# Performance work log

Measured on AMD Instinct MI355X. Metric: run time of the kernel, lower is better.

Reference implementation:

```python
import jax, jax.numpy as jnp
import numpy as np

N = 8192        # nodes
NFEAT = 256     # input feature dim
NHID = 64       # per-head hidden dim
NHEADS = 4
NCLASS = 121    # PPI label count
ALPHA = 0.2     # LeakyReLU negative slope
NEG_INF = jnp.float32(-9e15)  # pyGAT's mask fill value


def setup_inputs() -> dict:
    key = jax.random.key(0)
    k = jax.random.split(key, 6)
    x = jax.random.normal(k[0], (N, NFEAT), dtype=jnp.float32)
    adj = (jax.random.uniform(k[1], (N, N)) < 0.01).astype(jnp.float32)
    idx = jnp.arange(N)
    adj = adj.at[idx, idx].set(1.0)
    # per-head first-layer params: W [H, nfeat, nhid], a [H, 2*nhid]
    Ws = jax.random.normal(k[2], (NHEADS, NFEAT, NHID), dtype=jnp.float32) * 0.1
    a_heads = jax.random.normal(k[3], (NHEADS, 2 * NHID), dtype=jnp.float32) * 0.1
    # output attention layer params
    W_out = jax.random.normal(k[4], (NHEADS * NHID, NCLASS), dtype=jnp.float32) * 0.1
    a_out = jax.random.normal(k[5], (2 * NCLASS,), dtype=jnp.float32) * 0.1
    return {"x": x, "adj": adj, "Ws": Ws, "a_heads": a_heads,
            "W_out": W_out, "a_out": a_out}


def _gat_head(x, adj, W, a, concat):
    # Dense GraphAttentionLayer (pyGAT), eval mode (dropout off).
    Wh = x @ W                                   # [N, d]
    d = W.shape[1]
    f_src = Wh @ a[:d]                           # [N]  score contribution of node i
    f_dst = Wh @ a[d:]                           # [N]  score contribution of node j
    e = jax.nn.leaky_relu(f_src[:, None] + f_dst[None, :], ALPHA)  # [N, N]
    e = jnp.where(adj > 0, e, NEG_INF)
    att = jax.nn.softmax(e, axis=-1)             # [N, N]
    h = att @ Wh                                 # [N, d]
    return jax.nn.elu(h) if concat else h


def reference(x, adj, Ws, a_heads, W_out, a_out):
    # first multi-head layer (concat=True, elu), vmapped over heads
    heads = jax.vmap(lambda W, a: _gat_head(x, adj, W, a, True))(Ws, a_heads)  # [H, N, nhid]
    h_cat = jnp.transpose(heads, (1, 0, 2)).reshape(x.shape[0], NHEADS * NHID)  # torch.cat(dim=1)
    # output attention layer (concat=False -> raw aggregation)
    return _gat_head(h_cat, adj, W_out, a_out, False)  # [N, nclass]
```

## Files before the change

### kernel.cpp

```cpp
#include <hip/hip_runtime.h>
#include <math.h>

#define N_NODES 8192
#define NFEAT 256
#define NHID 64
#define NHEADS 4
#define NCLASS 121
#define NCPAD 128
#define CAP 256
#define LRALPHA 0.2f

__global__ __launch_bounds__(256) void build_csr(const float* __restrict__ adj,
                                                 int* __restrict__ nbr,
                                                 int* __restrict__ deg) {
    int row = blockIdx.x;
    __shared__ int cnt;
    if (threadIdx.x == 0) cnt = 0;
    __syncthreads();
    const float4* arow = (const float4*)(adj + (size_t)row * N_NODES);
    for (int j4 = threadIdx.x; j4 < N_NODES / 4; j4 += 256) {
        float4 v = arow[j4];
        if (v.x > 0.f) { int s = atomicAdd(&cnt, 1); if (s < CAP) nbr[row * CAP + s] = j4 * 4 + 0; }
        if (v.y > 0.f) { int s = atomicAdd(&cnt, 1); if (s < CAP) nbr[row * CAP + s] = j4 * 4 + 1; }
        if (v.z > 0.f) { int s = atomicAdd(&cnt, 1); if (s < CAP) nbr[row * CAP + s] = j4 * 4 + 2; }
        if (v.w > 0.f) { int s = atomicAdd(&cnt, 1); if (s < CAP) nbr[row * CAP + s] = j4 * 4 + 3; }
    }
    __syncthreads();
    if (threadIdx.x == 0) deg[row] = cnt < CAP ? cnt : CAP;
}

__global__ __launch_bounds__(256) void pad_params(const float* __restrict__ Wout,
                                                  const float* __restrict__ aout,
                                                  float* __restrict__ Wpad,
                                                  float* __restrict__ apad) {
    int idx = blockIdx.x * 256 + threadIdx.x;
    if (idx < 256 * NCPAD) {
        int k = idx >> 7, c = idx & 127;
        Wpad[idx] = (c < NCLASS) ? Wout[k * NCLASS + c] : 0.f;
    }
    if (idx < 256) {
        int c = idx & 127;
        float v = 0.f;
        if (c < NCLASS) v = (idx < 128) ? aout[c] : aout[NCLASS + c];
        apad[idx] = v;
    }
}

__global__ __launch_bounds__(256) void gemm1(const float* __restrict__ x,
                                             const float* __restrict__ Ws,
                                             float* __restrict__ Wh1) {
    int h = blockIdx.y;
    int r0 = blockIdx.x * 64;
    __shared__ float xs[64][260];
    for (int t = threadIdx.x; t < 64 * 64; t += 256) {
        int r = t >> 6, c4 = t & 63;
        *(float4*)&xs[r][c4 * 4] = *(const float4*)(x + (size_t)(r0 + r) * NFEAT + c4 * 4);
    }
    __syncthreads();
    int d = threadIdx.x & 63;
    int rb = (threadIdx.x >> 6) * 16;
    const float* W = Ws + (size_t)h * NFEAT * NHID + d;
    float acc[16] = {};
    for (int k4 = 0; k4 < NFEAT; k4 += 4) {
        float b0 = W[(k4 + 0) * NHID];
        float b1 = W[(k4 + 1) * NHID];
        float b2 = W[(k4 + 2) * NHID];
        float b3 = W[(k4 + 3) * NHID];
#pragma unroll
        for (int r = 0; r < 16; r++) {
            float4 a = *(const float4*)&xs[rb + r][k4];
            acc[r] += a.x * b0 + a.y * b1 + a.z * b2 + a.w * b3;
        }
    }
#pragma unroll
    for (int r = 0; r < 16; r++)
        Wh1[((size_t)(r0 + rb + r) * NHEADS + h) * NHID + d] = acc[r];
}

__global__ __launch_bounds__(256) void attn_coef1(const float* __restrict__ Wh1,
                                                  const float* __restrict__ a_heads,
                                                  float* __restrict__ fs1,
                                                  float* __restrict__ fd1) {
    int i = blockIdx.x;
    int h = threadIdx.x >> 6, lane = threadIdx.x & 63;
    float wh = Wh1[((size_t)i * NHEADS + h) * NHID + lane];
    float s = wh * a_heads[h * 2 * NHID + lane];
    float dd = wh * a_heads[h * 2 * NHID + NHID + lane];
#pragma unroll
    for (int o = 32; o > 0; o >>= 1) { s += __shfl_down(s, o); dd += __shfl_down(dd, o); }
    if (lane == 0) { fs1[h * N_NODES + i] = s; fd1[h * N_NODES + i] = dd; }
}

__global__ __launch_bounds__(256) void attn_agg1(const int* __restrict__ nbr,
                                                 const int* __restrict__ deg,
                                                 const float* __restrict__ Wh1,
                                                 const float* __restrict__ fs1,
                                                 const float* __restrict__ fd1,
                                                 float* __restrict__ hcat) {
    int i = blockIdx.x;
    int h = threadIdx.x >> 6, lane = threadIdx.x & 63;
    __shared__ float ebuf[NHEADS][CAP];
    __shared__ int nbrs[CAP];
    int dg = deg[i];
    for (int t = threadIdx.x; t < dg; t += 256) nbrs[t] = nbr[i * CAP + t];
    __syncthreads();
    float fsi = fs1[h * N_NODES + i];
    const float* fdh = fd1 + h * N_NODES;
    float m = -3.4e38f;
    for (int t = lane; t < dg; t += 64) {
        float e = fsi + fdh[nbrs[t]];
        e = e > 0.f ? e : LRALPHA * e;
        ebuf[h][t] = e;
        m = fmaxf(m, e);
    }
#pragma unroll
    for (int o = 32; o > 0; o >>= 1) m = fmaxf(m, __shfl_xor(m, o));
    float s = 0.f;
    for (int t = lane; t < dg; t += 64) {
        float p = __expf(ebuf[h][t] - m);
        ebuf[h][t] = p;
        s += p;
    }
#pragma unroll
    for (int o = 32; o > 0; o >>= 1) s += __shfl_xor(s, o);
    __syncthreads();
    float acc = 0.f;
    const float* whh = Wh1 + h * NHID + lane;
    for (int t = 0; t < dg; t++) {
        int j = nbrs[t];
        acc += ebuf[h][t] * whh[(size_t)j * (NHEADS * NHID)];
    }
    acc /= s;
    float r = acc > 0.f ? acc : expm1f(acc);
    hcat[(size_t)i * (NHEADS * NHID) + h * NHID + lane] = r;
}

__global__ __launch_bounds__(256) void gemm2(const float* __restrict__ hcat,
                                             const float* __restrict__ Wpad,
                                             float* __restrict__ Wh2) {
    int r0 = blockIdx.x * 64;
    __shared__ float xs[64][260];
    for (int t = threadIdx.x; t < 64 * 64; t += 256) {
        int r = t >> 6, c4 = t & 63;
        *(float4*)&xs[r][c4 * 4] = *(const float4*)(hcat + (size_t)(r0 + r) * 256 + c4 * 4);
    }
    __syncthreads();
    int c0 = (threadIdx.x & 63) * 2;
    int rb = (threadIdx.x >> 6) * 16;
    float acc0[16] = {}, acc1[16] = {};
    for (int k4 = 0; k4 < 256; k4 += 4) {
        float2 b0 = *(const float2*)&Wpad[(k4 + 0) * NCPAD + c0];
        float2 b1 = *(const float2*)&Wpad[(k4 + 1) * NCPAD + c0];
        float2 b2 = *(const float2*)&Wpad[(k4 + 2) * NCPAD + c0];
        float2 b3 = *(const float2*)&Wpad[(k4 + 3) * NCPAD + c0];
#pragma unroll
        for (int r = 0; r < 16; r++) {
            float4 a = *(const float4*)&xs[rb + r][k4];
            acc0[r] += a.x * b0.x + a.y * b1.x + a.z * b2.x + a.w * b3.x;
            acc1[r] += a.x * b0.y + a.y * b1.y + a.z * b2.y + a.w * b3.y;
        }
    }
#pragma unroll
    for (int r = 0; r < 16; r++) {
        float2 v = make_float2(acc0[r], acc1[r]);
        *(float2*)&Wh2[(size_t)(r0 + rb + r) * NCPAD + c0] = v;
    }
}

__global__ __launch_bounds__(256) void attn_coef2(const float* __restrict__ Wh2,
                                                  const float* __restrict__ apad,
                                                  float* __restrict__ fs2,
                                                  float* __restrict__ fd2) {
    int i = blockIdx.x * 4 + (threadIdx.x >> 6);
    int lane = threadIdx.x & 63;
    float w0 = Wh2[(size_t)i * NCPAD + lane];
    float w1 = Wh2[(size_t)i * NCPAD + 64 + lane];
    float s = w0 * apad[lane] + w1 * apad[64 + lane];
    float dd = w0 * apad[128 + lane] + w1 * apad[192 + lane];
#pragma unroll
    for (int o = 32; o > 0; o >>= 1) { s += __shfl_down(s, o); dd += __shfl_down(dd, o); }
    if (lane == 0) { fs2[i] = s; fd2[i] = dd; }
}

__global__ __launch_bounds__(128) void attn_agg2(const int* __restrict__ nbr,
                                                 const int* __restrict__ deg,
                                                 const float* __restrict__ Wh2,
                                                 const float* __restrict__ fs2,
                                                 const float* __restrict__ fd2,
                                                 float* __restrict__ out) {
    int i = blockIdx.x;
    int t = threadIdx.x;
    __shared__ float ebuf[CAP];
    __shared__ int nbrs[CAP];
    __shared__ float red[2];
    int dg = deg[i];
    for (int u = t; u < dg; u += 128) nbrs[u] = nbr[i * CAP + u];
    __syncthreads();
    float fsi = fs2[i];
    float m = -3.4e38f;
    for (int u = t; u < dg; u += 128) {
        float e = fsi + fd2[nbrs[u]];
        e = e > 0.f ? e : LRALPHA * e;
        ebuf[u] = e;
        m = fmaxf(m, e);
    }
#pragma unroll
    for (int o = 32; o > 0; o >>= 1) m = fmaxf(m, __shfl_xor(m, o));
    if ((t & 63) == 0) red[t >> 6] = m;
    __syncthreads();
    m = fmaxf(red[0], red[1]);
    float s = 0.f;
    for (int u = t; u < dg; u += 128) {
        float p = __expf(ebuf[u] - m);
        ebuf[u] = p;
        s += p;
    }
#pragma unroll
    for (int o = 32; o > 0; o >>= 1) s += __shfl_xor(s, o);
    __syncthreads();
    if ((t & 63) == 0) red[t >> 6] = s;
    __syncthreads();
    s = red[0] + red[1];
    float acc = 0.f;
    const float* wcol = Wh2 + t;
    for (int u = 0; u < dg; u++) {
        acc += ebuf[u] * wcol[(size_t)nbrs[u] * NCPAD];
    }
    if (t < NCLASS) out[(size_t)i * NCLASS + t] = acc / s;
}


extern "C" void kernel_launch(void* const* d_in, const int* in_sizes, int n_in,
                              void* d_out, int out_size, void* d_ws, size_t ws_size,
                              hipStream_t stream) {
    const float* x       = (const float*)d_in[0];
    const float* adj     = (const float*)d_in[1];
    const float* Ws      = (const float*)d_in[2];
    const float* a_heads = (const float*)d_in[3];
    const float* Wout    = (const float*)d_in[4];
    const float* aout    = (const float*)d_in[5];
    float* out = (float*)d_out;

    char* ws = (char*)d_ws;
    size_t off = 0;
    auto alloc = [&](size_t bytes) { void* p = ws + off; off = (off + bytes + 255) & ~(size_t)255; return p; };
    int*   nbr  = (int*)  alloc((size_t)N_NODES * CAP * 4);
    int*   deg  = (int*)  alloc((size_t)N_NODES * 4);
    float* Wh1  = (float*)alloc((size_t)N_NODES * NHEADS * NHID * 4);
    float* fs1  = (float*)alloc((size_t)NHEADS * N_NODES * 4);
    float* fd1  = (float*)alloc((size_t)NHEADS * N_NODES * 4);
    float* hcat = (float*)alloc((size_t)N_NODES * NHEADS * NHID * 4);
    float* Wh2  = (float*)alloc((size_t)N_NODES * NCPAD * 4);
    float* fs2  = (float*)alloc((size_t)N_NODES * 4);
    float* fd2  = (float*)alloc((size_t)N_NODES * 4);
    float* Wpad = (float*)alloc((size_t)256 * NCPAD * 4);
    float* apad = (float*)alloc((size_t)256 * 4);

    build_csr<<<N_NODES, 256, 0, stream>>>(adj, nbr, deg);
    pad_params<<<128, 256, 0, stream>>>(Wout, aout, Wpad, apad);
    gemm1<<<dim3(N_NODES / 64, NHEADS), 256, 0, stream>>>(x, Ws, Wh1);
    attn_coef1<<<N_NODES, 256, 0, stream>>>(Wh1, a_heads, fs1, fd1);
    attn_agg1<<<N_NODES, 256, 0, stream>>>(nbr, deg, Wh1, fs1, fd1, hcat);
    gemm2<<<N_NODES / 64, 256, 0, stream>>>(hcat, Wpad, Wh2);
    attn_coef2<<<N_NODES / 4, 256, 0, stream>>>(Wh2, apad, fs2, fd2);
    attn_agg2<<<N_NODES, 128, 0, stream>>>(nbr, deg, Wh2, fs2, fd2, out);
}
```

Measured before the change: 528.1 us.

## Store per-head feature matrices contiguously and remap aggregation blocks to one head

Wh1 and Wh2 are now stored head-major (and column-half-major for layer 2), so each gathered neighbour row is a contiguous 256-byte segment. The aggregation kernels are remapped so that each block covers four nodes for a single head or column half, with one wavefront per node. This keeps the gathered table for one head small enough to stay cache-resident. Non-temporal loads and stores are added for the adjacency scan, the neighbour lists and the outputs to reduce cache pollution. The cost is more redundant neighbour-list loads per node across heads, and the rewritten blocks depend on a correct block-index remapping.

Result: faster. 509.1 us (-3.6%).

```diff
diff --git a/kernel.cpp b/kernel.cpp
--- a/kernel.cpp
+++ b/kernel.cpp
@@ -10,6 +10,8 @@
 #define CAP 256
 #define LRALPHA 0.2f
 
+typedef float f32x4 __attribute__((ext_vector_type(4)));
+
 __global__ __launch_bounds__(256) void build_csr(const float* __restrict__ adj,
                                                  int* __restrict__ nbr,
                                                  int* __restrict__ deg) {
@@ -17,9 +19,9 @@
     __shared__ int cnt;
     if (threadIdx.x == 0) cnt = 0;
     __syncthreads();
-    const float4* arow = (const float4*)(adj + (size_t)row * N_NODES);
+    const f32x4* arow = (const f32x4*)(adj + (size_t)row * N_NODES);
     for (int j4 = threadIdx.x; j4 < N_NODES / 4; j4 += 256) {
-        float4 v = arow[j4];
+        f32x4 v = __builtin_nontemporal_load(&arow[j4]);
         if (v.x > 0.f) { int s = atomicAdd(&cnt, 1); if (s < CAP) nbr[row * CAP + s] = j4 * 4 + 0; }
         if (v.y > 0.f) { int s = atomicAdd(&cnt, 1); if (s < CAP) nbr[row * CAP + s] = j4 * 4 + 1; }
         if (v.z > 0.f) { int s = atomicAdd(&cnt, 1); if (s < CAP) nbr[row * CAP + s] = j4 * 4 + 2; }
@@ -48,7 +50,7 @@
 
 __global__ __launch_bounds__(256) void gemm1(const float* __restrict__ x,
                                              const float* __restrict__ Ws,
-                                             float* __restrict__ Wh1) {
+                                             float* __restrict__ Wh1h) {
     int h = blockIdx.y;
     int r0 = blockIdx.x * 64;
     __shared__ float xs[64][260];
@@ -74,16 +76,16 @@
     }
 #pragma unroll
     for (int r = 0; r < 16; r++)
-        Wh1[((size_t)(r0 + rb + r) * NHEADS + h) * NHID + d] = acc[r];
-}
-
-__global__ __launch_bounds__(256) void attn_coef1(const float* __restrict__ Wh1,
+        Wh1h[((size_t)h * N_NODES + (r0 + rb + r)) * NHID + d] = acc[r];
+}
+
+__global__ __launch_bounds__(256) void attn_coef1(const float* __restrict__ Wh1h,
                                                   const float* __restrict__ a_heads,
                                                   float* __restrict__ fs1,
                                                   float* __restrict__ fd1) {
     int i = blockIdx.x;
     int h = threadIdx.x >> 6, lane = threadIdx.x & 63;
-    float wh = Wh1[((size_t)i * NHEADS + h) * NHID + lane];
+    float wh = Wh1h[((size_t)h * N_NODES + i) * NHID + lane];
     float s = wh * a_heads[h * 2 * NHID + lane];
     float dd = wh * a_heads[h * 2 * NHID + NHID + lane];
 #pragma unroll
@@ -93,51 +95,55 @@
 
 __global__ __launch_bounds__(256) void attn_agg1(const int* __restrict__ nbr,
                                                  const int* __restrict__ deg,
-                                                 const float* __restrict__ Wh1,
+                                                 const float* __restrict__ Wh1h,
                                                  const float* __restrict__ fs1,
                                                  const float* __restrict__ fd1,
                                                  float* __restrict__ hcat) {
-    int i = blockIdx.x;
-    int h = threadIdx.x >> 6, lane = threadIdx.x & 63;
-    __shared__ float ebuf[NHEADS][CAP];
-    __shared__ int nbrs[CAP];
+    int b = blockIdx.x;
+    int w = threadIdx.x >> 6, lane = threadIdx.x & 63;
+    int slot = b & 7;
+    int h = slot >> 1;
+    int g = ((b >> 3) << 1) | (slot & 1);
+    int i = (g << 2) | w;
+    __shared__ float ebuf[4][CAP];
+    __shared__ int nbrs[4][CAP];
     int dg = deg[i];
-    for (int t = threadIdx.x; t < dg; t += 256) nbrs[t] = nbr[i * CAP + t];
-    __syncthreads();
+    for (int t = lane; t < dg; t += 64)
+        nbrs[w][t] = __builtin_nontemporal_load(&nbr[i * CAP + t]);
     float fsi = fs1[h * N_NODES + i];
     const float* fdh = fd1 + h * N_NODES;
     float m = -3.4e38f;
     for (int t = lane; t < dg; t += 64) {
-        float e = fsi + fdh[nbrs[t]];
+        float e = fsi + fdh[nbrs[w][t]];
         e = e > 0.f ? e : LRALPHA * e;
-        ebuf[h][t] = e;
+        ebuf[w][t] = e;
         m = fmaxf(m, e);
     }
 #pragma unroll
     for (int o = 32; o > 0; o >>= 1) m = fmaxf(m, __shfl_xor(m, o));
     float s = 0.f;
     for (int t = lane; t < dg; t += 64) {
-        float p = __expf(ebuf[h][t] - m);
-        ebuf[h][t] = p;
+        float p = __expf(ebuf[w][t] - m);
+        ebuf[w][t] = p;
         s += p;
     }
 #pragma unroll
     for (int o = 32; o > 0; o >>= 1) s += __shfl_xor(s, o);
     __syncthreads();
     float acc = 0.f;
-    const float* whh = Wh1 + h * NHID + lane;
+    const float* wcol = Wh1h + (size_t)h * N_NODES * NHID + lane;
+#pragma unroll 4
     for (int t = 0; t < dg; t++) {
-        int j = nbrs[t];
-        acc += ebuf[h][t] * whh[(size_t)j * (NHEADS * NHID)];
+        acc += ebuf[w][t] * wcol[(size_t)nbrs[w][t] * NHID];
     }
     acc /= s;
     float r = acc > 0.f ? acc : expm1f(acc);
-    hcat[(size_t)i * (NHEADS * NHID) + h * NHID + lane] = r;
+    __builtin_nontemporal_store(r, &hcat[(size_t)i * (NHEADS * NHID) + h * NHID + lane]);
 }
 
 __global__ __launch_bounds__(256) void gemm2(const float* __restrict__ hcat,
                                              const float* __restrict__ Wpad,
-                                             float* __restrict__ Wh2) {
+                                             float* __restrict__ Wh2h) {
     int r0 = blockIdx.x * 64;
     __shared__ float xs[64][260];
     for (int t = threadIdx.x; t < 64 * 64; t += 256) {
@@ -147,6 +153,7 @@
     __syncthreads();
     int c0 = (threadIdx.x & 63) * 2;
     int rb = (threadIdx.x >> 6) * 16;
+    int half = c0 >> 6, cc = c0 & 63;
     float acc0[16] = {}, acc1[16] = {};
     for (int k4 = 0; k4 < 256; k4 += 4) {
         float2 b0 = *(const float2*)&Wpad[(k4 + 0) * NCPAD + c0];
@@ -163,18 +170,18 @@
 #pragma unroll
     for (int r = 0; r < 16; r++) {
         float2 v = make_float2(acc0[r], acc1[r]);
-        *(float2*)&Wh2[(size_t)(r0 + rb + r) * NCPAD + c0] = v;
-    }
-}
-
-__global__ __launch_bounds__(256) void attn_coef2(const float* __restrict__ Wh2,
+        *(float2*)&Wh2h[((size_t)half * N_NODES + (r0 + rb + r)) * 64 + cc] = v;
+    }
+}
+
+__global__ __launch_bounds__(256) void attn_coef2(const float* __restrict__ Wh2h,
                                                   const float* __restrict__ apad,
                                                   float* __restrict__ fs2,
                                                   float* __restrict__ fd2) {
     int i = blockIdx.x * 4 + (threadIdx.x >> 6);
     int lane = threadIdx.x & 63;
-    float w0 = Wh2[(size_t)i * NCPAD + lane];
-    float w1 = Wh2[(size_t)i * NCPAD + 64 + lane];
+    float w0 = Wh2h[(size_t)i * 64 + lane];
+    float w1 = Wh2h[((size_t)N_NODES + i) * 64 + lane];
     float s = w0 * apad[lane] + w1 * apad[64 + lane];
     float dd = w0 * apad[128 + lane] + w1 * apad[192 + lane];
 #pragma unroll
@@ -182,51 +189,51 @@
     if (lane == 0) { fs2[i] = s; fd2[i] = dd; }
 }
 
-__global__ __launch_bounds__(128) void attn_agg2(const int* __restrict__ nbr,
+__global__ __launch_bounds__(256) void attn_agg2(const int* __restrict__ nbr,
                                                  const int* __restrict__ deg,
-                                                 const float* __restrict__ Wh2,
+                                                 const float* __restrict__ Wh2h,
                                                  const float* __restrict__ fs2,
                                                  const float* __restrict__ fd2,
                                                  float* __restrict__ out) {
-    int i = blockIdx.x;
-    int t = threadIdx.x;
-    __shared__ float ebuf[CAP];
-    __shared__ int nbrs[CAP];
-    __shared__ float red[2];
+    int b = blockIdx.x;
+    int w = threadIdx.x >> 6, lane = threadIdx.x & 63;
+    int slot = b & 7;
+    int hf = slot >> 2;
+    int g = ((b >> 3) << 2) | (slot & 3);
+    int i = (g << 2) | w;
+    __shared__ float ebuf[4][CAP];
+    __shared__ int nbrs[4][CAP];
     int dg = deg[i];
-    for (int u = t; u < dg; u += 128) nbrs[u] = nbr[i * CAP + u];
-    __syncthreads();
+    for (int t = lane; t < dg; t += 64)
+        nbrs[w][t] = __builtin_nontemporal_load(&nbr[i * CAP + t]);
     float fsi = fs2[i];
     float m = -3.4e38f;
-    for (int u = t; u < dg; u += 128) {
-        float e = fsi + fd2[nbrs[u]];
+    for (int t = lane; t < dg; t += 64) {
+        float e = fsi + fd2[nbrs[w][t]];
         e = e > 0.f ? e : LRALPHA * e;
-        ebuf[u] = e;
+        ebuf[w][t] = e;
         m = fmaxf(m, e);
     }
 #pragma unroll
     for (int o = 32; o > 0; o >>= 1) m = fmaxf(m, __shfl_xor(m, o));
-    if ((t & 63) == 0) red[t >> 6] = m;
-    __syncthreads();
-    m = fmaxf(red[0], red[1]);
     float s = 0.f;
-    for (int u = t; u < dg; u += 128) {
-        float p = __expf(ebuf[u] - m);
-        ebuf[u] = p;
+    for (int t = lane; t < dg; t += 64) {
+        float p = __expf(ebuf[w][t] - m);
+        ebuf[w][t] = p;
         s += p;
     }
 #pragma unroll
     for (int o = 32; o > 0; o >>= 1) s += __shfl_xor(s, o);
     __syncthreads();
-    if ((t & 63) == 0) red[t >> 6] = s;
-    __syncthreads();
-    s = red[0] + red[1];
     float acc = 0.f;
-    const float* wcol = Wh2 + t;
-    for (int u = 0; u < dg; u++) {
-        acc += ebuf[u] * wcol[(size_t)nbrs[u] * NCPAD];
-    }
-    if (t < NCLASS) out[(size_t)i * NCLASS + t] = acc / s;
+    const float* wcol = Wh2h + (size_t)hf * N_NODES * 64 + lane;
+#pragma unroll 4
+    for (int t = 0; t < dg; t++) {
+        acc += ebuf[w][t] * wcol[(size_t)nbrs[w][t] * 64];
+    }
+    int c = hf * 64 + lane;
+    if (c < NCLASS)
+        __builtin_nontemporal_store(acc / s, &out[(size_t)i * NCLASS + c]);
 }
 
 
@@ -246,11 +253,11 @@
     auto alloc = [&](size_t bytes) { void* p = ws + off; off = (off + bytes + 255) & ~(size_t)255; return p; };
     int*   nbr  = (int*)  alloc((size_t)N_NODES * CAP * 4);
     int*   deg  = (int*)  alloc((size_t)N_NODES * 4);
-    float* Wh1  = (float*)alloc((size_t)N_NODES * NHEADS * NHID * 4);
+    float* Wh1h = (float*)alloc((size_t)NHEADS * N_NODES * NHID * 4);
     float* fs1  = (float*)alloc((size_t)NHEADS * N_NODES * 4);
     float* fd1  = (float*)alloc((size_t)NHEADS * N_NODES * 4);
     float* hcat = (float*)alloc((size_t)N_NODES * NHEADS * NHID * 4);
-    float* Wh2  = (float*)alloc((size_t)N_NODES * NCPAD * 4);
+    float* Wh2h = (float*)alloc((size_t)2 * N_NODES * 64 * 4);
     float* fs2  = (float*)alloc((size_t)N_NODES * 4);
     float* fd2  = (float*)alloc((size_t)N_NODES * 4);
     float* Wpad = (float*)alloc((size_t)256 * NCPAD * 4);
@@ -258,10 +265,10 @@
 
     build_csr<<<N_NODES, 256, 0, stream>>>(adj, nbr, deg);
     pad_params<<<128, 256, 0, stream>>>(Wout, aout, Wpad, apad);
-    gemm1<<<dim3(N_NODES / 64, NHEADS), 256, 0, stream>>>(x, Ws, Wh1);
-    attn_coef1<<<N_NODES, 256, 0, stream>>>(Wh1, a_heads, fs1, fd1);
-    attn_agg1<<<N_NODES, 256, 0, stream>>>(nbr, deg, Wh1, fs1, fd1, hcat);
-    gemm2<<<N_NODES / 64, 256, 0, stream>>>(hcat, Wpad, Wh2);
-    attn_coef2<<<N_NODES / 4, 256, 0, stream>>>(Wh2, apad, fs2, fd2);
-    attn_agg2<<<N_NODES, 128, 0, stream>>>(nbr, deg, Wh2, fs2, fd2, out);
-}
+    gemm1<<<dim3(N_NODES / 64, NHEADS), 256, 0, stream>>>(x, Ws, Wh1h);
+    attn_coef1<<<N_NODES, 256, 0, stream>>>(Wh1h, a_heads, fs1, fd1);
+    attn_agg1<<<N_NODES, 256, 0, stream>>>(nbr, deg, Wh1h, fs1, fd1, hcat);
+    gemm2<<<N_NODES / 64, 256, 0, stream>>>(hcat, Wpad, Wh2h);
+    attn_coef2<<<N_NODES / 4, 256, 0, stream>>>(Wh2h, apad, fs2, fd2);
+    attn_agg2<<<N_NODES / 2, 256, 0, stream>>>(nbr, deg, Wh2h, fs2, fd2, out);
+}
```

## Restructure attention aggregation to one wavefront per node with vectorized gathers

Applied to the files above, without the earlier changes.

Both aggregation kernels now give each 64-lane wavefront one node (four nodes per block) instead of one block per node. The first layer handles all four heads at once, using head-interleaved fs/fd arrays and float4 gathers of neighbor features. The output layer splits neighbors across two half-waves that combine with a shuffle. The adjacency scan in build_csr uses nontemporal loads. The intent is to cut block-level syncs, raise memory-level parallelism and use wider loads in the gather-bound phases. The cost is more register pressure and a hard limit of four neighbor chunks per lane, which matches CAP=256.

Result: faster. 485.2 us (-8.1%).

```diff
diff --git a/kernel.cpp b/kernel.cpp
--- a/kernel.cpp
+++ b/kernel.cpp
@@ -10,6 +10,11 @@
 #define CAP 256
 #define LRALPHA 0.2f
 
+typedef float f32x4 __attribute__((ext_vector_type(4)));
+
+__device__ __forceinline__ float lrelu(float x) { return x > 0.f ? x : LRALPHA * x; }
+__device__ __forceinline__ f32x4 splat4(float v) { f32x4 r = {v, v, v, v}; return r; }
+
 __global__ __launch_bounds__(256) void build_csr(const float* __restrict__ adj,
                                                  int* __restrict__ nbr,
                                                  int* __restrict__ deg) {
@@ -17,9 +22,9 @@
     __shared__ int cnt;
     if (threadIdx.x == 0) cnt = 0;
     __syncthreads();
-    const float4* arow = (const float4*)(adj + (size_t)row * N_NODES);
+    const f32x4* arow = (const f32x4*)(adj + (size_t)row * N_NODES);
     for (int j4 = threadIdx.x; j4 < N_NODES / 4; j4 += 256) {
-        float4 v = arow[j4];
+        f32x4 v = __builtin_nontemporal_load(&arow[j4]);
         if (v.x > 0.f) { int s = atomicAdd(&cnt, 1); if (s < CAP) nbr[row * CAP + s] = j4 * 4 + 0; }
         if (v.y > 0.f) { int s = atomicAdd(&cnt, 1); if (s < CAP) nbr[row * CAP + s] = j4 * 4 + 1; }
         if (v.z > 0.f) { int s = atomicAdd(&cnt, 1); if (s < CAP) nbr[row * CAP + s] = j4 * 4 + 2; }
@@ -74,65 +79,101 @@
     }
 #pragma unroll
     for (int r = 0; r < 16; r++)
-        Wh1[((size_t)(r0 + rb + r) * NHEADS + h) * NHID + d] = acc[r];
+        Wh1[(size_t)(r0 + rb + r) * (NHEADS * NHID) + h * NHID + d] = acc[r];
 }
 
 __global__ __launch_bounds__(256) void attn_coef1(const float* __restrict__ Wh1,
                                                   const float* __restrict__ a_heads,
-                                                  float* __restrict__ fs1,
-                                                  float* __restrict__ fd1) {
+                                                  float* __restrict__ fs1t,
+                                                  float* __restrict__ fd1t) {
     int i = blockIdx.x;
     int h = threadIdx.x >> 6, lane = threadIdx.x & 63;
-    float wh = Wh1[((size_t)i * NHEADS + h) * NHID + lane];
+    float wh = Wh1[(size_t)i * (NHEADS * NHID) + h * NHID + lane];
     float s = wh * a_heads[h * 2 * NHID + lane];
     float dd = wh * a_heads[h * 2 * NHID + NHID + lane];
 #pragma unroll
     for (int o = 32; o > 0; o >>= 1) { s += __shfl_down(s, o); dd += __shfl_down(dd, o); }
-    if (lane == 0) { fs1[h * N_NODES + i] = s; fd1[h * N_NODES + i] = dd; }
+    if (lane == 0) { fs1t[i * 4 + h] = s; fd1t[i * 4 + h] = dd; }
 }
 
 __global__ __launch_bounds__(256) void attn_agg1(const int* __restrict__ nbr,
                                                  const int* __restrict__ deg,
                                                  const float* __restrict__ Wh1,
-                                                 const float* __restrict__ fs1,
-                                                 const float* __restrict__ fd1,
+                                                 const float* __restrict__ fs1t,
+                                                 const float* __restrict__ fd1t,
                                                  float* __restrict__ hcat) {
-    int i = blockIdx.x;
-    int h = threadIdx.x >> 6, lane = threadIdx.x & 63;
-    __shared__ float ebuf[NHEADS][CAP];
-    __shared__ int nbrs[CAP];
+    int w = threadIdx.x >> 6, lane = threadIdx.x & 63;
+    int i = blockIdx.x * 4 + w;
+    __shared__ int nbrs[4][CAP];
+    __shared__ float pbuf[4][CAP][4];
     int dg = deg[i];
-    for (int t = threadIdx.x; t < dg; t += 256) nbrs[t] = nbr[i * CAP + t];
-    __syncthreads();
-    float fsi = fs1[h * N_NODES + i];
-    const float* fdh = fd1 + h * N_NODES;
-    float m = -3.4e38f;
-    for (int t = lane; t < dg; t += 64) {
-        float e = fsi + fdh[nbrs[t]];
-        e = e > 0.f ? e : LRALPHA * e;
-        ebuf[h][t] = e;
-        m = fmaxf(m, e);
-    }
-#pragma unroll
-    for (int o = 32; o > 0; o >>= 1) m = fmaxf(m, __shfl_xor(m, o));
-    float s = 0.f;
-    for (int t = lane; t < dg; t += 64) {
-        float p = __expf(ebuf[h][t] - m);
-        ebuf[h][t] = p;
-        s += p;
-    }
-#pragma unroll
-    for (int o = 32; o > 0; o >>= 1) s += __shfl_xor(s, o);
-    __syncthreads();
-    float acc = 0.f;
-    const float* whh = Wh1 + h * NHID + lane;
+    for (int t = lane; t < dg; t += 64)
+        nbrs[w][t] = nbr[i * CAP + t];
+    f32x4 fsi = *(const f32x4*)(fs1t + (size_t)i * 4);
+    f32x4 e[4];
+    f32x4 m4 = {-3.4e38f, -3.4e38f, -3.4e38f, -3.4e38f};
+#pragma unroll
+    for (int k = 0; k < 4; k++) {
+        int t = lane + (k << 6);
+        if (t < dg) {
+            int j = nbrs[w][t];
+            f32x4 fdj = *(const f32x4*)(fd1t + (size_t)j * 4);
+            f32x4 ev;
+            ev.x = lrelu(fsi.x + fdj.x);
+            ev.y = lrelu(fsi.y + fdj.y);
+            ev.z = lrelu(fsi.z + fdj.z);
+            ev.w = lrelu(fsi.w + fdj.w);
+            e[k] = ev;
+            m4.x = fmaxf(m4.x, ev.x); m4.y = fmaxf(m4.y, ev.y);
+            m4.z = fmaxf(m4.z, ev.z); m4.w = fmaxf(m4.w, ev.w);
+        }
+    }
+#pragma unroll
+    for (int o = 32; o > 0; o >>= 1) {
+        m4.x = fmaxf(m4.x, __shfl_xor(m4.x, o));
+        m4.y = fmaxf(m4.y, __shfl_xor(m4.y, o));
+        m4.z = fmaxf(m4.z, __shfl_xor(m4.z, o));
+        m4.w = fmaxf(m4.w, __shfl_xor(m4.w, o));
+    }
+    f32x4 s4 = {0.f, 0.f, 0.f, 0.f};
+#pragma unroll
+    for (int k = 0; k < 4; k++) {
+        int t = lane + (k << 6);
+        if (t < dg) {
+            f32x4 p;
+            p.x = __expf(e[k].x - m4.x);
+            p.y = __expf(e[k].y - m4.y);
+            p.z = __expf(e[k].z - m4.z);
+            p.w = __expf(e[k].w - m4.w);
+            *(f32x4*)&pbuf[w][t][0] = p;
+            s4 += p;
+        }
+    }
+#pragma unroll
+    for (int o = 32; o > 0; o >>= 1) {
+        s4.x += __shfl_xor(s4.x, o);
+        s4.y += __shfl_xor(s4.y, o);
+        s4.z += __shfl_xor(s4.z, o);
+        s4.w += __shfl_xor(s4.w, o);
+    }
+    __syncthreads();
+    int hl = lane >> 4;
+    const float* wrow = Wh1 + 4 * lane;
+    f32x4 acc = {0.f, 0.f, 0.f, 0.f};
+#pragma unroll 4
     for (int t = 0; t < dg; t++) {
-        int j = nbrs[t];
-        acc += ebuf[h][t] * whh[(size_t)j * (NHEADS * NHID)];
-    }
-    acc /= s;
-    float r = acc > 0.f ? acc : expm1f(acc);
-    hcat[(size_t)i * (NHEADS * NHID) + h * NHID + lane] = r;
+        int j = nbrs[w][t];
+        float p = pbuf[w][t][hl];
+        f32x4 wv = *(const f32x4*)(wrow + (size_t)j * (NHEADS * NHID));
+        acc += wv * splat4(p);
+    }
+    float sh = hl == 0 ? s4.x : hl == 1 ? s4.y : hl == 2 ? s4.z : s4.w;
+    acc.x /= sh; acc.y /= sh; acc.z /= sh; acc.w /= sh;
+    acc.x = acc.x > 0.f ? acc.x : expm1f(acc.x);
+    acc.y = acc.y > 0.f ? acc.y : expm1f(acc.y);
+    acc.z = acc.z > 0.f ? acc.z : expm1f(acc.z);
+    acc.w = acc.w > 0.f ? acc.w : expm1f(acc.w);
+    *(f32x4*)(hcat + (size_t)i * (NHEADS * NHID) + 4 * lane) = acc;
 }
 
 __global__ __launch_bounds__(256) void gemm2(const float* __restrict__ hcat,
@@ -182,51 +223,67 @@
     if (lane == 0) { fs2[i] = s; fd2[i] = dd; }
 }
 
-__global__ __launch_bounds__(128) void attn_agg2(const int* __restrict__ nbr,
+__global__ __launch_bounds__(256) void attn_agg2(const int* __restrict__ nbr,
                                                  const int* __restrict__ deg,
                                                  const float* __restrict__ Wh2,
                                                  const float* __restrict__ fs2,
                                                  const float* __restrict__ fd2,
                                                  float* __restrict__ out) {
-    int i = blockIdx.x;
-    int t = threadIdx.x;
-    __shared__ float ebuf[CAP];
-    __shared__ int nbrs[CAP];
-    __shared__ float red[2];
+    int w = threadIdx.x >> 6, lane = threadIdx.x & 63;
+    int i = blockIdx.x * 4 + w;
+    __shared__ int nbrs[4][CAP];
+    __shared__ float pbuf[4][CAP];
     int dg = deg[i];
-    for (int u = t; u < dg; u += 128) nbrs[u] = nbr[i * CAP + u];
-    __syncthreads();
+    for (int t = lane; t < dg; t += 64)
+        nbrs[w][t] = nbr[i * CAP + t];
     float fsi = fs2[i];
+    float e[4];
     float m = -3.4e38f;
-    for (int u = t; u < dg; u += 128) {
-        float e = fsi + fd2[nbrs[u]];
-        e = e > 0.f ? e : LRALPHA * e;
-        ebuf[u] = e;
-        m = fmaxf(m, e);
+#pragma unroll
+    for (int k = 0; k < 4; k++) {
+        int t = lane + (k << 6);
+        if (t < dg) {
+            float ev = lrelu(fsi + fd2[nbrs[w][t]]);
+            e[k] = ev;
+            m = fmaxf(m, ev);
+        }
     }
 #pragma unroll
     for (int o = 32; o > 0; o >>= 1) m = fmaxf(m, __shfl_xor(m, o));
-    if ((t & 63) == 0) red[t >> 6] = m;
-    __syncthreads();
-    m = fmaxf(red[0], red[1]);
     float s = 0.f;
-    for (int u = t; u < dg; u += 128) {
-        float p = __expf(ebuf[u] - m);
-        ebuf[u] = p;
-        s += p;
+#pragma unroll
+    for (int k = 0; k < 4; k++) {
+        int t = lane + (k << 6);
+        if (t < dg) {
+            float p = __expf(e[k] - m);
+            pbuf[w][t] = p;
+            s += p;
+        }
     }
 #pragma unroll
     for (int o = 32; o > 0; o >>= 1) s += __shfl_xor(s, o);
     __syncthreads();
-    if ((t & 63) == 0) red[t >> 6] = s;
-    __syncthreads();
-    s = red[0] + red[1];
-    float acc = 0.f;
-    const float* wcol = Wh2 + t;
-    for (int u = 0; u < dg; u++) {
-        acc += ebuf[u] * wcol[(size_t)nbrs[u] * NCPAD];
-    }
-    if (t < NCLASS) out[(size_t)i * NCLASS + t] = acc / s;
+    int eg = lane >> 5, c = lane & 31;
+    const float* wrow = Wh2 + 4 * c;
+    f32x4 acc = {0.f, 0.f, 0.f, 0.f};
+    for (int tt = 0; tt < dg; tt += 2) {
+        int t = tt + eg;
+        int tc = t < dg ? t : 0;
+        float p = t < dg ? pbuf[w][tc] : 0.f;
+        int j = nbrs[w][tc];
+        f32x4 wv = *(const f32x4*)(wrow + (size_t)j * NCPAD);
+        acc += wv * splat4(p);
+    }
+    acc.x += __shfl_xor(acc.x, 32);
+    acc.y += __shfl_xor(acc.y, 32);
+    acc.z += __shfl_xor(acc.z, 32);
+    acc.w += __shfl_xor(acc.w, 32);
+    if (eg == 0) {
+        int c4 = c * 4;
+#pragma unroll
+        for (int q = 0; q < 4; q++)
+            if (c4 + q < NCLASS) out[(size_t)i * NCLASS + c4 + q] = acc[q] / s;
+    }
 }
 
 
@@ -247,8 +304,8 @@
     int*   nbr  = (int*)  alloc((size_t)N_NODES * CAP * 4);
     int*   deg  = (int*)  alloc((size_t)N_NODES * 4);
     float* Wh1  = (float*)alloc((size_t)N_NODES * NHEADS * NHID * 4);
-    float* fs1  = (float*)alloc((size_t)NHEADS * N_NODES * 4);
-    float* fd1  = (float*)alloc((size_t)NHEADS * N_NODES * 4);
+    float* fs1t = (float*)alloc((size_t)N_NODES * 4 * 4);
+    float* fd1t = (float*)alloc((size_t)N_NODES * 4 * 4);
     float* hcat = (float*)alloc((size_t)N_NODES * NHEADS * NHID * 4);
     float* Wh2  = (float*)alloc((size_t)N_NODES * NCPAD * 4);
     float* fs2  = (float*)alloc((size_t)N_NODES * 4);
@@ -259,9 +316,9 @@
     build_csr<<<N_NODES, 256, 0, stream>>>(adj, nbr, deg);
     pad_params<<<128, 256, 0, stream>>>(Wout, aout, Wpad, apad);
     gemm1<<<dim3(N_NODES / 64, NHEADS), 256, 0, stream>>>(x, Ws, Wh1);
-    attn_coef1<<<N_NODES, 256, 0, stream>>>(Wh1, a_heads, fs1, fd1);
-    attn_agg1<<<N_NODES, 256, 0, stream>>>(nbr, deg, Wh1, fs1, fd1, hcat);
+    attn_coef1<<<N_NODES, 256, 0, stream>>>(Wh1, a_heads, fs1t, fd1t);
+    attn_agg1<<<N_NODES / 4, 256, 0, stream>>>(nbr, deg, Wh1, fs1t, fd1t, hcat);
     gemm2<<<N_NODES / 64, 256, 0, stream>>>(hcat, Wpad, Wh2);
     attn_coef2<<<N_NODES / 4, 256, 0, stream>>>(Wh2, apad, fs2, fd2);
-    attn_agg2<<<N_NODES, 128, 0, stream>>>(nbr, deg, Wh2, fs2, fd2, out);
-}
+    attn_agg2<<<N_NODES / 4, 256, 0, stream>>>(nbr, deg, Wh2, fs2, fd2, out);
+}
```
